# Kernel tuning notes

Hardware: AMD Instinct MI355X
Metric: run time of the kernel (lower is better)

Reference implementation:

```python
import jax, jax.numpy as jnp
import numpy as np
import math

B, T, C = 4, 2048, 1024
H, D = 16, 64  # n_head, head_dim; H*D == C

def setup_inputs() -> dict:
    key = jax.random.key(0)
    ks = jax.random.split(key, 8)
    s = 1.0 / math.sqrt(C)
    return {
        "x": jax.random.normal(ks[0], (B, T, C), jnp.float32),
        "W_attn": jax.random.normal(ks[1], (C, 3 * C), jnp.float32) * s,
        "b_attn": jax.random.normal(ks[2], (3 * C,), jnp.float32) * 0.02,
        "W_proj": jax.random.normal(ks[3], (C, C), jnp.float32) * s,
        "b_proj": jax.random.normal(ks[4], (C,), jnp.float32) * 0.02,
        "bQ": jax.random.normal(ks[5], (H, D), jnp.float32) * 0.02,
        "bK": jax.random.normal(ks[6], (H, D), jnp.float32) * 0.02,
        "bV": jax.random.normal(ks[7], (H, D), jnp.float32) * 0.02,
    }

def reference(x, W_attn, b_attn, W_proj, b_proj, bQ, bK, bV):
    Bx, Tx, Cx = x.shape
    qkv = x @ W_attn + b_attn                       # [B,T,3C]
    q, k, v = jnp.split(qkv, 3, axis=-1)
    def heads(t):
        return t.reshape(Bx, Tx, H, D).transpose(0, 2, 1, 3)  # [B,H,T,D]
    q = heads(q) + bQ[None, :, None, :]
    k = heads(k) + bK[None, :, None, :]
    v = heads(v) + bV[None, :, None, :]
    scale = 1.0 / math.sqrt(D)
    scores = jnp.einsum('bhqd,bhkd->bhqk', q, k) * scale      # [B,H,T,T]
    causal = jnp.tril(jnp.ones((Tx, Tx), dtype=bool))
    scores = jnp.where(causal[None, None], scores, -jnp.inf)
    att = jax.nn.softmax(scores, axis=-1)
    y = jnp.einsum('bhqk,bhkd->bhqd', att, v)                 # [B,H,T,D]
    y = y.transpose(0, 2, 1, 3).reshape(Bx, Tx, Cx)
    return y @ W_proj + b_proj
```

## Files before the change

kernel.cpp:

```cpp
#include <hip/hip_runtime.h>
#include <hip/hip_bf16.h>

#define BB 4
#define TT 2048
#define CC 1024
#define HH 16
#define DD 64

typedef __bf16 bf16x8 __attribute__((ext_vector_type(8)));
typedef float f32x4 __attribute__((ext_vector_type(4)));
typedef unsigned int u32x4 __attribute__((ext_vector_type(4)));
typedef unsigned short u16x8 __attribute__((ext_vector_type(8)));
typedef unsigned short u16x4 __attribute__((ext_vector_type(4)));
typedef unsigned int u32;

__device__ __forceinline__ unsigned short f2bf(float f) {
  u32 u = __builtin_bit_cast(u32, f);
  u += 0x7fff + ((u >> 16) & 1);
  return (unsigned short)(u >> 16);
}

__device__ __forceinline__ bf16x8 lds_load8(const unsigned short* p) {
  u32x4 t = *(const u32x4*)p;
  return __builtin_bit_cast(bf16x8, t);
}

__device__ __forceinline__ void g2l16(const unsigned short* g, unsigned short* l) {
  __builtin_amdgcn_global_load_lds(
      (const __attribute__((address_space(1))) u32*)g,
      (__attribute__((address_space(3))) u32*)l, 16, 0, 0);
}

__global__ __launch_bounds__(256) void xcast(const float* __restrict__ x,
                                             unsigned short* __restrict__ xb) {
  int i = (blockIdx.x * 256 + threadIdx.x) * 8;
  f32x4 a = *(const f32x4*)(x + i);
  f32x4 b = *(const f32x4*)(x + i + 4);
  u16x8 o;
  o[0] = f2bf(a[0]); o[1] = f2bf(a[1]); o[2] = f2bf(a[2]); o[3] = f2bf(a[3]);
  o[4] = f2bf(b[0]); o[5] = f2bf(b[1]); o[6] = f2bf(b[2]); o[7] = f2bf(b[3]);
  *(u16x8*)(xb + i) = o;
}

__global__ __launch_bounds__(256) void wtrans(const float* __restrict__ W,
                                              unsigned short* __restrict__ Wt, int N) {
  __shared__ unsigned short T[64 * 68];
  const int tid = threadIdx.x;
  const int n0 = blockIdx.x * 64, k0 = blockIdx.y * 64;
#pragma unroll
  for (int it = 0; it < 4; ++it) {
    int idx = it * 256 + tid;
    int kk = idx >> 4, nn = (idx & 15) * 4;
    f32x4 v = *(const f32x4*)(W + (size_t)(k0 + kk) * N + n0 + nn);
    u16x4 p;
    p[0] = f2bf(v[0]); p[1] = f2bf(v[1]); p[2] = f2bf(v[2]); p[3] = f2bf(v[3]);
    *(u16x4*)(&T[kk * 68 + nn]) = p;
  }
  __syncthreads();
#pragma unroll
  for (int it = 0; it < 4; ++it) {
    int idx = it * 256 + tid;
    int nn = idx >> 4, kc = (idx & 15) * 4;
    u16x4 o;
    o[0] = T[(kc + 0) * 68 + nn];
    o[1] = T[(kc + 1) * 68 + nn];
    o[2] = T[(kc + 2) * 68 + nn];
    o[3] = T[(kc + 3) * 68 + nn];
    *(u16x4*)(Wt + (size_t)(n0 + nn) * 1024 + k0 + kc) = o;
  }
}

__global__ __launch_bounds__(256) void qkv_gemm(
    const unsigned short* __restrict__ xb, const unsigned short* __restrict__ Wt,
    const float* __restrict__ b_attn, const float* __restrict__ bQ,
    const float* __restrict__ bK, const float* __restrict__ bV,
    unsigned short* __restrict__ Qb, unsigned short* __restrict__ Kb,
    unsigned short* __restrict__ Vb)
{
  __shared__ unsigned short Al[128 * 32];
  __shared__ unsigned short Bl[128 * 32];
  const int tid = threadIdx.x;
  const int w = tid >> 6, lane = tid & 63;
  const int l16 = lane & 15, quad = lane >> 4;
  const int nblk = blockIdx.x % 24, mblk = blockIdx.x / 24;
  const int m0 = mblk * 128, n0 = nblk * 128;
  const int wm = (w & 1) * 64, wn = (w >> 1) * 64;

  const unsigned short* ga = xb + (size_t)(m0 + w * 16 + (lane >> 2)) * 1024 + (lane & 3) * 8;
  const unsigned short* gb = Wt + (size_t)(n0 + w * 16 + (lane >> 2)) * 1024 + (lane & 3) * 8;
  unsigned short* la = &Al[w * 512];
  unsigned short* lb = &Bl[w * 512];

  f32x4 acc[4][4] = {};

  for (int kb = 0; kb < 1024; kb += 32) {
    __syncthreads();
    g2l16(ga + kb, la);
    g2l16(ga + kb + 65536, la + 2048);
    g2l16(gb + kb, lb);
    g2l16(gb + kb + 65536, lb + 2048);
    __syncthreads();
    bf16x8 af[4], bfr[4];
#pragma unroll
    for (int mi = 0; mi < 4; ++mi)
      af[mi] = lds_load8(&Al[(wm + mi * 16 + l16) * 32 + quad * 8]);
#pragma unroll
    for (int ni = 0; ni < 4; ++ni)
      bfr[ni] = lds_load8(&Bl[(wn + ni * 16 + l16) * 32 + quad * 8]);
#pragma unroll
    for (int mi = 0; mi < 4; ++mi)
#pragma unroll
      for (int ni = 0; ni < 4; ++ni)
        acc[mi][ni] = __builtin_amdgcn_mfma_f32_16x16x32_bf16(
            af[mi], bfr[ni], acc[mi][ni], 0, 0, 0);
  }

  unsigned short* dst[4];
  float biasv[4], sc[4];
  int st[4];
#pragma unroll
  for (int ni = 0; ni < 4; ++ni) {
    int col = n0 + wn + ni * 16 + l16;
    int sec = col >> 10, cc = col & 1023;
    const float* hb = (sec == 0) ? bQ : (sec == 1 ? bK : bV);
    biasv[ni] = b_attn[col] + hb[cc];
    sc[ni] = (sec == 0) ? 0.125f * 1.44269504f : 1.0f;
    if (sec == 2) {
      dst[ni] = Vb + (size_t)(cc >> 6) * (DD * TT) + (size_t)(cc & 63) * TT;
      st[ni] = 1;
    } else {
      unsigned short* base = (sec == 0) ? Qb : Kb;
      dst[ni] = base + (size_t)(cc >> 6) * (TT * DD) + (cc & 63);
      st[ni] = 64;
    }
  }
#pragma unroll
  for (int mi = 0; mi < 4; ++mi)
#pragma unroll
    for (int r = 0; r < 4; ++r) {
      int m = m0 + wm + mi * 16 + quad * 4 + r;
      int bidx = m >> 11, t = m & 2047;
      size_t co = (size_t)bidx * (HH * TT * DD);
#pragma unroll
      for (int ni = 0; ni < 4; ++ni)
        dst[ni][co + (size_t)t * st[ni]] = f2bf((acc[mi][ni][r] + biasv[ni]) * sc[ni]);
    }
}

__global__ __launch_bounds__(256) void attn_kernel(
    const unsigned short* __restrict__ Qb, const unsigned short* __restrict__ Kb,
    const unsigned short* __restrict__ Vtg, unsigned short* __restrict__ Yb)
{
  __shared__ unsigned short Kl[64 * 64];
  __shared__ unsigned short Vl[64 * 64];
  __shared__ unsigned short Pl[4 * 32 * 72];
  const int tid = threadIdx.x;
  const int w = tid >> 6, lane = tid & 63;
  const int l16 = lane & 15, quad = lane >> 4;
  const int qt = 15 - (blockIdx.x >> 6);
  const int bh = blockIdx.x & 63;
  const int b = bh >> 4, h = bh & 15;
  const int q0 = qt * 128, qw = q0 + w * 32;

  const unsigned short* Qg = Qb + (size_t)bh * TT * DD;
  const unsigned short* Kg = Kb + (size_t)bh * TT * DD;
  const unsigned short* Vg = Vtg + (size_t)bh * DD * TT;

  bf16x8 qf[2][2];
#pragma unroll
  for (int mi = 0; mi < 2; ++mi)
#pragma unroll
    for (int dk = 0; dk < 2; ++dk) {
      u32x4 t = *(const u32x4*)(Qg + (size_t)(qw + mi * 16 + l16) * 64 + dk * 32 + quad * 8);
      qf[mi][dk] = __builtin_bit_cast(bf16x8, t);
    }

  f32x4 accO[2][4] = {};
  f32x4 accL[2] = {};
  u16x8 o16;
#pragma unroll
  for (int j = 0; j < 8; ++j) o16[j] = 0x3F80;
  const bf16x8 onesf = __builtin_bit_cast(bf16x8, o16);

  const int srow = w * 8 + (lane >> 3);
  const int schunk = ((lane & 7) ^ (srow & 7)) * 8;
  const int kkey = 4 * (srow & 15) + (srow >> 4);
  const unsigned short* gk1 = Kg + (size_t)kkey * 64 + schunk;
  const unsigned short* gk2 = Kg + (size_t)(kkey + 2) * 64 + schunk;
  const unsigned short* gv1 = Vg + (size_t)srow * TT + schunk;
  const unsigned short* gv2 = Vg + (size_t)(srow + 32) * TT + schunk;
  unsigned short* klw = &Kl[w * 512];
  unsigned short* vlw = &Vl[w * 512];

  const int kend = q0 + 64;
  for (int k0 = 0; k0 <= kend; k0 += 64) {
    __syncthreads();
    g2l16(gk1 + (size_t)k0 * 64, klw);
    g2l16(gk2 + (size_t)k0 * 64, klw + 2048);
    g2l16(gv1 + k0, vlw);
    g2l16(gv2 + k0, vlw + 2048);
    __syncthreads();
    if (k0 > qw + 31) continue;

    f32x4 accS[2][4] = {};
#pragma unroll
    for (int ni = 0; ni < 4; ++ni)
#pragma unroll
      for (int dk = 0; dk < 2; ++dk) {
        bf16x8 kf = lds_load8(
            &Kl[(ni * 16 + l16) * 64 + (((dk * 4 + quad) ^ (l16 & 7)) * 8)]);
#pragma unroll
        for (int mi = 0; mi < 2; ++mi)
          accS[mi][ni] = __builtin_amdgcn_mfma_f32_16x16x32_bf16(
              qf[mi][dk], kf, accS[mi][ni], 0, 0, 0);
      }

    const bool maskT = (k0 + 63 > qw);
#pragma unroll
    for (int mi = 0; mi < 2; ++mi)
#pragma unroll
      for (int r = 0; r < 4; ++r) {
        int qrow = qw + mi * 16 + quad * 4 + r;
        float s0 = accS[mi][0][r], s1 = accS[mi][1][r];
        float s2 = accS[mi][2][r], s3 = accS[mi][3][r];
        if (maskT) {
          int kb = k0 + 4 * l16;
          if (kb + 0 > qrow) s0 = -3e38f;
          if (kb + 1 > qrow) s1 = -3e38f;
          if (kb + 2 > qrow) s2 = -3e38f;
          if (kb + 3 > qrow) s3 = -3e38f;
        }
        u16x4 pk;
        pk[0] = f2bf(exp2f(s0));
        pk[1] = f2bf(exp2f(s1));
        pk[2] = f2bf(exp2f(s2));
        pk[3] = f2bf(exp2f(s3));
        *(u16x4*)(&Pl[(w * 32 + mi * 16 + quad * 4 + r) * 72 + 4 * l16]) = pk;
      }

#pragma unroll
    for (int kc = 0; kc < 2; ++kc) {
      bf16x8 pf[2];
#pragma unroll
      for (int mi = 0; mi < 2; ++mi)
        pf[mi] = lds_load8(&Pl[(w * 32 + mi * 16 + l16) * 72 + kc * 32 + quad * 8]);
#pragma unroll
      for (int dn = 0; dn < 4; ++dn) {
        bf16x8 vf = lds_load8(
            &Vl[(dn * 16 + l16) * 64 + (((kc * 4 + quad) ^ (l16 & 7)) * 8)]);
#pragma unroll
        for (int mi = 0; mi < 2; ++mi)
          accO[mi][dn] = __builtin_amdgcn_mfma_f32_16x16x32_bf16(
              pf[mi], vf, accO[mi][dn], 0, 0, 0);
      }
#pragma unroll
      for (int mi = 0; mi < 2; ++mi)
        accL[mi] = __builtin_amdgcn_mfma_f32_16x16x32_bf16(
            pf[mi], onesf, accL[mi], 0, 0, 0);
    }
  }

#pragma unroll
  for (int mi = 0; mi < 2; ++mi)
#pragma unroll
    for (int r = 0; r < 4; ++r) {
      int q = qw + mi * 16 + quad * 4 + r;
      float inv = 1.0f / accL[mi][r];
      size_t base = ((size_t)b * TT + q) * CC + h * DD;
#pragma unroll
      for (int dn = 0; dn < 4; ++dn)
        Yb[base + dn * 16 + l16] = f2bf(accO[mi][dn][r] * inv);
    }
}

__global__ __launch_bounds__(256) void proj_gemm(
    const unsigned short* __restrict__ Yb, const unsigned short* __restrict__ Wt,
    const float* __restrict__ bp, float* __restrict__ out)
{
  __shared__ unsigned short Al[128 * 32];
  __shared__ unsigned short Bl[128 * 32];
  const int tid = threadIdx.x;
  const int w = tid >> 6, lane = tid & 63;
  const int l16 = lane & 15, quad = lane >> 4;
  const int nblk = blockIdx.x & 7, mblk = blockIdx.x >> 3;
  const int m0 = mblk * 128, n0 = nblk * 128;
  const int wm = (w & 1) * 64, wn = (w >> 1) * 64;

  const unsigned short* ga = Yb + (size_t)(m0 + w * 16 + (lane >> 2)) * 1024 + (lane & 3) * 8;
  const unsigned short* gb = Wt + (size_t)(n0 + w * 16 + (lane >> 2)) * 1024 + (lane & 3) * 8;
  unsigned short* la = &Al[w * 512];
  unsigned short* lb = &Bl[w * 512];

  f32x4 acc[4][4] = {};

  for (int kb = 0; kb < 1024; kb += 32) {
    __syncthreads();
    g2l16(ga + kb, la);
    g2l16(ga + kb + 65536, la + 2048);
    g2l16(gb + kb, lb);
    g2l16(gb + kb + 65536, lb + 2048);
    __syncthreads();
    bf16x8 af[4], bfr[4];
#pragma unroll
    for (int mi = 0; mi < 4; ++mi)
      af[mi] = lds_load8(&Al[(wm + mi * 16 + l16) * 32 + quad * 8]);
#pragma unroll
    for (int ni = 0; ni < 4; ++ni)
      bfr[ni] = lds_load8(&Bl[(wn + ni * 16 + l16) * 32 + quad * 8]);
#pragma unroll
    for (int mi = 0; mi < 4; ++mi)
#pragma unroll
      for (int ni = 0; ni < 4; ++ni)
        acc[mi][ni] = __builtin_amdgcn_mfma_f32_16x16x32_bf16(
            af[mi], bfr[ni], acc[mi][ni], 0, 0, 0);
  }

#pragma unroll
  for (int mi = 0; mi < 4; ++mi)
#pragma unroll
    for (int r = 0; r < 4; ++r) {
      int m = m0 + wm + mi * 16 + quad * 4 + r;
#pragma unroll
      for (int ni = 0; ni < 4; ++ni) {
        int c = n0 + wn + ni * 16 + l16;
        out[(size_t)m * 1024 + c] = acc[mi][ni][r] + bp[c];
      }
    }
}

extern "C" void kernel_launch(void* const* d_in, const int* in_sizes, int n_in,
                              void* d_out, int out_size, void* d_ws, size_t ws_size,
                              hipStream_t stream) {
  const float* x      = (const float*)d_in[0];
  const float* W_attn = (const float*)d_in[1];
  const float* b_attn = (const float*)d_in[2];
  const float* W_proj = (const float*)d_in[3];
  const float* b_proj = (const float*)d_in[4];
  const float* bQ     = (const float*)d_in[5];
  const float* bK     = (const float*)d_in[6];
  const float* bV     = (const float*)d_in[7];
  float* out = (float*)d_out;

  unsigned short* xb   = (unsigned short*)d_ws;
  unsigned short* Yb   = xb;
  unsigned short* Wt_a = xb + 8388608;
  unsigned short* Wt_p = Wt_a + 3145728;
  unsigned short* Qb   = Wt_p + 1048576;
  unsigned short* Kb   = Qb + 8388608;
  unsigned short* Vb   = Kb + 8388608;

  xcast<<<dim3(4096), dim3(256), 0, stream>>>(x, xb);
  wtrans<<<dim3(48, 16), dim3(256), 0, stream>>>(W_attn, Wt_a, 3072);
  wtrans<<<dim3(16, 16), dim3(256), 0, stream>>>(W_proj, Wt_p, 1024);
  qkv_gemm<<<dim3(64 * 24), dim3(256), 0, stream>>>(xb, Wt_a, b_attn, bQ, bK, bV,
                                                    Qb, Kb, Vb);
  attn_kernel<<<dim3(16 * 64), dim3(256), 0, stream>>>(Qb, Kb, Vb, Yb);
  proj_gemm<<<dim3(64 * 8), dim3(256), 0, stream>>>(Yb, Wt_p, b_proj, out);
}
```

Baseline: 299.4 us.

## Widen GEMM K-tile to 64 with XOR-swizzled LDS, fuse prep kernels, truncate P

Both GEMMs now stage 64-wide K tiles with an XOR-swizzled LDS layout, which halves the number of barrier pairs per K sweep and is meant to avoid LDS bank conflicts on fragment reads. The cast kernel and the two weight-transpose kernels are merged into a single launch to save launch overhead. In the attention kernel, P values are packed to bf16 by truncation with v_perm instead of round-to-nearest, which lowers VALU cost but slightly reduces precision. The larger LDS tiles may lower occupancy.

```diff
diff --git a/kernel.cpp b/kernel.cpp
--- a/kernel.cpp
+++ b/kernel.cpp
@@ -10,6 +10,7 @@
 typedef __bf16 bf16x8 __attribute__((ext_vector_type(8)));
 typedef float f32x4 __attribute__((ext_vector_type(4)));
 typedef unsigned int u32x4 __attribute__((ext_vector_type(4)));
+typedef unsigned int u32x2 __attribute__((ext_vector_type(2)));
 typedef unsigned short u16x8 __attribute__((ext_vector_type(8)));
 typedef unsigned short u16x4 __attribute__((ext_vector_type(4)));
 typedef unsigned int u32;
@@ -31,22 +32,32 @@
       (__attribute__((address_space(3))) u32*)l, 16, 0, 0);
 }
 
-__global__ __launch_bounds__(256) void xcast(const float* __restrict__ x,
-                                             unsigned short* __restrict__ xb) {
-  int i = (blockIdx.x * 256 + threadIdx.x) * 8;
-  f32x4 a = *(const f32x4*)(x + i);
-  f32x4 b = *(const f32x4*)(x + i + 4);
-  u16x8 o;
-  o[0] = f2bf(a[0]); o[1] = f2bf(a[1]); o[2] = f2bf(a[2]); o[3] = f2bf(a[3]);
-  o[4] = f2bf(b[0]); o[5] = f2bf(b[1]); o[6] = f2bf(b[2]); o[7] = f2bf(b[3]);
-  *(u16x8*)(xb + i) = o;
-}
-
-__global__ __launch_bounds__(256) void wtrans(const float* __restrict__ W,
-                                              unsigned short* __restrict__ Wt, int N) {
+__global__ __launch_bounds__(256) void prep(
+    const float* __restrict__ x, const float* __restrict__ Wa,
+    const float* __restrict__ Wp, unsigned short* __restrict__ xb,
+    unsigned short* __restrict__ Wta, unsigned short* __restrict__ Wtp)
+{
   __shared__ unsigned short T[64 * 68];
   const int tid = threadIdx.x;
-  const int n0 = blockIdx.x * 64, k0 = blockIdx.y * 64;
+  const int bid = blockIdx.x;
+  if (bid < 4096) {
+    int i = (bid * 256 + tid) * 8;
+    f32x4 a = *(const f32x4*)(x + i);
+    f32x4 b = *(const f32x4*)(x + i + 4);
+    u16x8 o;
+    o[0] = f2bf(a[0]); o[1] = f2bf(a[1]); o[2] = f2bf(a[2]); o[3] = f2bf(a[3]);
+    o[4] = f2bf(b[0]); o[5] = f2bf(b[1]); o[6] = f2bf(b[2]); o[7] = f2bf(b[3]);
+    *(u16x8*)(xb + i) = o;
+    return;
+  }
+  const float* W; unsigned short* Wt; int N, n0, k0;
+  if (bid < 4096 + 768) {
+    int b2 = bid - 4096;  W = Wa; Wt = Wta; N = 3072;
+    n0 = (b2 % 48) * 64;  k0 = (b2 / 48) * 64;
+  } else {
+    int b2 = bid - 4864;  W = Wp; Wt = Wtp; N = 1024;
+    n0 = (b2 % 16) * 64;  k0 = (b2 / 16) * 64;
+  }
 #pragma unroll
   for (int it = 0; it < 4; ++it) {
     int idx = it * 256 + tid;
@@ -77,8 +88,8 @@
     unsigned short* __restrict__ Qb, unsigned short* __restrict__ Kb,
     unsigned short* __restrict__ Vb)
 {
-  __shared__ unsigned short Al[128 * 32];
-  __shared__ unsigned short Bl[128 * 32];
+  __shared__ unsigned short Al[128 * 64];
+  __shared__ unsigned short Bl[128 * 64];
   const int tid = threadIdx.x;
   const int w = tid >> 6, lane = tid & 63;
   const int l16 = lane & 15, quad = lane >> 4;
@@ -86,33 +97,45 @@
   const int m0 = mblk * 128, n0 = nblk * 128;
   const int wm = (w & 1) * 64, wn = (w >> 1) * 64;
 
-  const unsigned short* ga = xb + (size_t)(m0 + w * 16 + (lane >> 2)) * 1024 + (lane & 3) * 8;
-  const unsigned short* gb = Wt + (size_t)(n0 + w * 16 + (lane >> 2)) * 1024 + (lane & 3) * 8;
-  unsigned short* la = &Al[w * 512];
-  unsigned short* lb = &Bl[w * 512];
+  const int srow = lane >> 3;
+  const int schunk = ((lane & 7) ^ (srow & 7)) * 8;
+  const unsigned short* ga = xb + (size_t)(m0 + w * 8 + srow) * 1024 + schunk;
+  const unsigned short* gb = Wt + (size_t)(n0 + w * 8 + srow) * 1024 + schunk;
+  unsigned short* la = &Al[(w * 8) * 64];
+  unsigned short* lb = &Bl[(w * 8) * 64];
 
   f32x4 acc[4][4] = {};
 
-  for (int kb = 0; kb < 1024; kb += 32) {
-    __syncthreads();
-    g2l16(ga + kb, la);
-    g2l16(ga + kb + 65536, la + 2048);
-    g2l16(gb + kb, lb);
-    g2l16(gb + kb + 65536, lb + 2048);
-    __syncthreads();
-    bf16x8 af[4], bfr[4];
+  for (int kb = 0; kb < 1024; kb += 64) {
+    __syncthreads();
+#pragma unroll
+    for (int i = 0; i < 4; ++i) {
+      g2l16(ga + kb + (size_t)i * 32 * 1024, la + i * 32 * 64);
+      g2l16(gb + kb + (size_t)i * 32 * 1024, lb + i * 32 * 64);
+    }
+    __syncthreads();
+    bf16x8 af[4][2], bfr[4][2];
 #pragma unroll
     for (int mi = 0; mi < 4; ++mi)
-      af[mi] = lds_load8(&Al[(wm + mi * 16 + l16) * 32 + quad * 8]);
+#pragma unroll
+      for (int dk = 0; dk < 2; ++dk)
+        af[mi][dk] = lds_load8(
+            &Al[(wm + mi * 16 + l16) * 64 + (((dk * 4 + quad) ^ (l16 & 7)) * 8)]);
 #pragma unroll
     for (int ni = 0; ni < 4; ++ni)
-      bfr[ni] = lds_load8(&Bl[(wn + ni * 16 + l16) * 32 + quad * 8]);
+#pragma unroll
+      for (int dk = 0; dk < 2; ++dk)
+        bfr[ni][dk] = lds_load8(
+            &Bl[(wn + ni * 16 + l16) * 64 + (((dk * 4 + quad) ^ (l16 & 7)) * 8)]);
 #pragma unroll
     for (int mi = 0; mi < 4; ++mi)
 #pragma unroll
-      for (int ni = 0; ni < 4; ++ni)
+      for (int ni = 0; ni < 4; ++ni) {
         acc[mi][ni] = __builtin_amdgcn_mfma_f32_16x16x32_bf16(
-            af[mi], bfr[ni], acc[mi][ni], 0, 0, 0);
+            af[mi][0], bfr[ni][0], acc[mi][ni], 0, 0, 0);
+        acc[mi][ni] = __builtin_amdgcn_mfma_f32_16x16x32_bf16(
+            af[mi][1], bfr[ni][1], acc[mi][ni], 0, 0, 0);
+      }
   }
 
   unsigned short* dst[4];
@@ -230,12 +253,14 @@
           if (kb + 2 > qrow) s2 = -3e38f;
           if (kb + 3 > qrow) s3 = -3e38f;
         }
-        u16x4 pk;
-        pk[0] = f2bf(exp2f(s0));
-        pk[1] = f2bf(exp2f(s1));
-        pk[2] = f2bf(exp2f(s2));
-        pk[3] = f2bf(exp2f(s3));
-        *(u16x4*)(&Pl[(w * 32 + mi * 16 + quad * 4 + r) * 72 + 4 * l16]) = pk;
+        u32 e0 = __builtin_bit_cast(u32, exp2f(s0));
+        u32 e1 = __builtin_bit_cast(u32, exp2f(s1));
+        u32 e2 = __builtin_bit_cast(u32, exp2f(s2));
+        u32 e3 = __builtin_bit_cast(u32, exp2f(s3));
+        u32x2 pv;
+        pv[0] = __builtin_amdgcn_perm(e1, e0, 0x07060302);
+        pv[1] = __builtin_amdgcn_perm(e3, e2, 0x07060302);
+        *(u32x2*)(&Pl[(w * 32 + mi * 16 + quad * 4 + r) * 72 + 4 * l16]) = pv;
       }
 
 #pragma unroll
@@ -277,8 +302,8 @@
     const unsigned short* __restrict__ Yb, const unsigned short* __restrict__ Wt,
     const float* __restrict__ bp, float* __restrict__ out)
 {
-  __shared__ unsigned short Al[128 * 32];
-  __shared__ unsigned short Bl[128 * 32];
+  __shared__ unsigned short Al[128 * 64];
+  __shared__ unsigned short Bl[128 * 64];
   const int tid = threadIdx.x;
   const int w = tid >> 6, lane = tid & 63;
   const int l16 = lane & 15, quad = lane >> 4;
@@ -286,33 +311,45 @@
   const int m0 = mblk * 128, n0 = nblk * 128;
   const int wm = (w & 1) * 64, wn = (w >> 1) * 64;
 
-  const unsigned short* ga = Yb + (size_t)(m0 + w * 16 + (lane >> 2)) * 1024 + (lane & 3) * 8;
-  const unsigned short* gb = Wt + (size_t)(n0 + w * 16 + (lane >> 2)) * 1024 + (lane & 3) * 8;
-  unsigned short* la = &Al[w * 512];
-  unsigned short* lb = &Bl[w * 512];
+  const int srow = lane >> 3;
+  const int schunk = ((lane & 7) ^ (srow & 7)) * 8;
+  const unsigned short* ga = Yb + (size_t)(m0 + w * 8 + srow) * 1024 + schunk;
+  const unsigned short* gb = Wt + (size_t)(n0 + w * 8 + srow) * 1024 + schunk;
+  unsigned short* la = &Al[(w * 8) * 64];
+  unsigned short* lb = &Bl[(w * 8) * 64];
 
   f32x4 acc[4][4] = {};
 
-  for (int kb = 0; kb < 1024; kb += 32) {
-    __syncthreads();
-    g2l16(ga + kb, la);
-    g2l16(ga + kb + 65536, la + 2048);
-    g2l16(gb + kb, lb);
-    g2l16(gb + kb + 65536, lb + 2048);
-    __syncthreads();
-    bf16x8 af[4], bfr[4];
+  for (int kb = 0; kb < 1024; kb += 64) {
+    __syncthreads();
+#pragma unroll
+    for (int i = 0; i < 4; ++i) {
+      g2l16(ga + kb + (size_t)i * 32 * 1024, la + i * 32 * 64);
+      g2l16(gb + kb + (size_t)i * 32 * 1024, lb + i * 32 * 64);
+    }
+    __syncthreads();
+    bf16x8 af[4][2], bfr[4][2];
 #pragma unroll
     for (int mi = 0; mi < 4; ++mi)
-      af[mi] = lds_load8(&Al[(wm + mi * 16 + l16) * 32 + quad * 8]);
+#pragma unroll
+      for (int dk = 0; dk < 2; ++dk)
+        af[mi][dk] = lds_load8(
+            &Al[(wm + mi * 16 + l16) * 64 + (((dk * 4 + quad) ^ (l16 & 7)) * 8)]);
 #pragma unroll
     for (int ni = 0; ni < 4; ++ni)
-      bfr[ni] = lds_load8(&Bl[(wn + ni * 16 + l16) * 32 + quad * 8]);
+#pragma unroll
+      for (int dk = 0; dk < 2; ++dk)
+        bfr[ni][dk] = lds_load8(
+            &Bl[(wn + ni * 16 + l16) * 64 + (((dk * 4 + quad) ^ (l16 & 7)) * 8)]);
 #pragma unroll
     for (int mi = 0; mi < 4; ++mi)
 #pragma unroll
-      for (int ni = 0; ni < 4; ++ni)
+      for (int ni = 0; ni < 4; ++ni) {
         acc[mi][ni] = __builtin_amdgcn_mfma_f32_16x16x32_bf16(
-            af[mi], bfr[ni], acc[mi][ni], 0, 0, 0);
+            af[mi][0], bfr[ni][0], acc[mi][ni], 0, 0, 0);
+        acc[mi][ni] = __builtin_amdgcn_mfma_f32_16x16x32_bf16(
+            af[mi][1], bfr[ni][1], acc[mi][ni], 0, 0, 0);
+      }
   }
 
 #pragma unroll
@@ -349,9 +386,8 @@
   unsigned short* Kb   = Qb + 8388608;
   unsigned short* Vb   = Kb + 8388608;
 
-  xcast<<<dim3(4096), dim3(256), 0, stream>>>(x, xb);
-  wtrans<<<dim3(48, 16), dim3(256), 0, stream>>>(W_attn, Wt_a, 3072);
-  wtrans<<<dim3(16, 16), dim3(256), 0, stream>>>(W_proj, Wt_p, 1024);
+  prep<<<dim3(4096 + 768 + 256), dim3(256), 0, stream>>>(x, W_attn, W_proj,
+                                                         xb, Wt_a, Wt_p);
   qkv_gemm<<<dim3(64 * 24), dim3(256), 0, stream>>>(xb, Wt_a, b_attn, bQ, bK, bV,
                                                     Qb, Kb, Vb);
   attn_kernel<<<dim3(16 * 64), dim3(256), 0, stream>>>(Qb, Kb, Vb, Yb);
```

Result: faster. 280.1 us (-6.4%).
